# Performance work log

Hardware: AMD Instinct MI355X
Metric: run time of the kernel (lower is better)

The kernel has to match this reference:

```python
import jax, jax.numpy as jnp
import numpy as np

G, NPG = 2048, 512          # glimpses, points per glimpse
N0 = G * NPG                # 1,048,576 input points
CPG, CPG2 = 128, 32         # clusters per glimpse at level1/level2
M1, M2 = G * CPG, G * CPG2  # 262144, 65536


def _seg_mean_np(x, ids, m):
    cnt = np.bincount(ids, minlength=m).astype(np.float32)
    out = np.stack([np.bincount(ids, weights=x[:, d], minlength=m) for d in range(x.shape[1])], axis=1)
    return (out / np.maximum(cnt, 1.0)[:, None]).astype(np.float32)


def setup_inputs() -> dict:
    key = jax.random.key(0)
    ks = jax.random.split(key, 16)
    rng = np.random.default_rng(0)
    pos_np = (rng.random((N0, 3)) * 4.0).astype(np.float32)
    # voxel_mean_pool level 0: each point -> a cluster within its glimpse
    g_of_pt = np.arange(N0) // NPG
    out_index0 = (g_of_pt * CPG + rng.integers(0, CPG, N0)).astype(np.int64)
    pos1_np = _seg_mean_np(pos_np, out_index0, M1)
    g_of_c1 = np.arange(M1) // CPG
    out_index1 = (g_of_c1 * CPG2 + rng.integers(0, CPG2, M1)).astype(np.int64)
    pos2_np = _seg_mean_np(pos1_np, out_index1, M2)
    out_index2 = (np.arange(M2) // CPG2).astype(np.int64)  # glimpse id per level-2 point

    def w(k, shp, s=0.05):
        return jax.random.normal(k, shp, dtype=jnp.float32) * s

    return {
        "rgb": jax.random.normal(ks[0], (N0, 1), dtype=jnp.float32),
        "pos": jnp.asarray(pos_np), "pos1": jnp.asarray(pos1_np), "pos2": jnp.asarray(pos2_np),
        "out_index0": jnp.asarray(out_index0), "out_index1": jnp.asarray(out_index1),
        "out_index2": jnp.asarray(out_index2),
        "eps": jax.random.normal(ks[1], (G, 128), dtype=jnp.float32),
        # conv1: local (c_in=1 + 3 -> 16), global (16 -> 32)
        "W1l": w(ks[2], (4, 16)), "b1l": jnp.zeros(16), "W1g": w(ks[3], (16, 32)), "b1g": jnp.zeros(32),
        # conv2: (32+3 -> 64), (64 -> 128)
        "W2l": w(ks[4], (35, 64)), "b2l": jnp.zeros(64), "W2g": w(ks[5], (64, 128)), "b2g": jnp.zeros(128),
        # conv3: (128+3 -> 128), (128 -> 256)
        "W3l": w(ks[6], (131, 128)), "b3l": jnp.zeros(128), "W3g": w(ks[7], (128, 256)), "b3g": jnp.zeros(256),
        "Wlin": w(ks[8], (256, 256)), "blin": jnp.zeros(256),
    }


def _point_conv(x_in, pos_in, pos_out, out_index, Wl, bl, Wg, bg):
    # gather relative position of each input point w.r.t. its output center
    rel = pos_in - pos_out[out_index]                      # [E,3]
    h = jax.nn.celu(jnp.concatenate([x_in, rel], -1) @ Wl + bl)  # per-edge MLP
    m = pos_out.shape[0]
    cnt = jax.ops.segment_sum(jnp.ones((h.shape[0],), h.dtype), out_index, num_segments=m)
    agg = jax.ops.segment_sum(h, out_index, num_segments=m) / jnp.maximum(cnt, 1.0)[:, None]
    return agg @ Wg + bg


def reference(rgb, pos, pos1, pos2, out_index0, out_index1, out_index2, eps,
              W1l, b1l, W1g, b1g, W2l, b2l, W2g, b2g, W3l, b3l, W3g, b3g, Wlin, blin):
    f = rgb  # ar=False path: feature = rgb
    f = jax.nn.celu(_point_conv(f, pos, pos1, out_index0, W1l, b1l, W1g, b1g))   # [M1,32]
    f = jax.nn.celu(_point_conv(f, pos1, pos2, out_index1, W2l, b2l, W2g, b2g))  # [M2,128]
    centers = jnp.zeros((G, 3), f.dtype)  # pos_sample = zeros_like(glimpse__center)
    f = jax.nn.celu(_point_conv(f, pos2, centers, out_index2, W3l, b3l, W3g, b3g))  # [G,256]
    out = f @ Wlin + blin
    mu, sg = jnp.split(out, 2, axis=1)
    sigma = jax.nn.softplus(sg)  # to_sigma
    z = mu + sigma * eps         # Normal.rsample
    z_what, z_mask = jnp.split(z, 2, axis=1)
    return z_what, z_mask, mu, sigma, f
```

## Files before the change

### kernel.cpp

```cpp
#include <hip/hip_runtime.h>
#include <hip/hip_bf16.h>
#include <cstddef>

#define G_   2048
#define NPG_ 512
#define CPG_ 128
#define CPG2_ 32

#define OFF_ZW 0
#define OFF_ZM (G_*64)
#define OFF_MU (2*G_*64)
#define OFF_SG (2*G_*64 + G_*128)
#define OFF_F  (2*G_*64 + 2*G_*128)

typedef __attribute__((ext_vector_type(8))) short bf16x8;
typedef __attribute__((ext_vector_type(4))) float f32x4;

__device__ __forceinline__ float celu_f(float x)     { return x > 0.f ? x : __expf(x) - 1.f; }
__device__ __forceinline__ float softplus_f(float x) { return fmaxf(x, 0.f) + __logf(1.f + __expf(-fabsf(x))); }
__device__ __forceinline__ unsigned short f2bf(float x) {
    __hip_bfloat16 h = __float2bfloat16(x);
    return *reinterpret_cast<unsigned short*>(&h);
}
__device__ __forceinline__ float bflo(unsigned w) { return __uint_as_float(w << 16); }
__device__ __forceinline__ float bfhi(unsigned w) { return __uint_as_float(w & 0xffff0000u); }

__global__ void k_prep(const float* __restrict__ W2l, const float* __restrict__ W2g,
                       const float* __restrict__ W3l, const float* __restrict__ W3g,
                       const float* __restrict__ Wlin,
                       unsigned short* __restrict__ w2lT, unsigned short* __restrict__ w2gT,
                       unsigned short* __restrict__ w3lT, unsigned short* __restrict__ w3gT,
                       unsigned short* __restrict__ wlinT)
{
    const int tid = blockIdx.x*256 + threadIdx.x, stride = gridDim.x*256;
    for (int i = tid; i < 64*64; i += stride) {
        const int ch = i >> 6, k = i & 63;
        w2lT[i] = f2bf(k < 35 ? W2l[k*64 + ch] : 0.f);
    }
    for (int i = tid; i < 128*64; i += stride) {
        const int ch = i >> 6, k = i & 63;
        w2gT[i] = f2bf(W2g[k*128 + ch]);
    }
    for (int i = tid; i < 128*160; i += stride) {
        const int ch = i / 160, k = i % 160;
        w3lT[i] = f2bf(k < 131 ? W3l[k*128 + ch] : 0.f);
    }
    for (int i = tid; i < 256*128; i += stride) {
        const int ch = i >> 7, k = i & 127;
        w3gT[i] = f2bf(W3g[k*256 + ch]);
    }
    for (int i = tid; i < 256*256; i += stride) {
        const int ch = i >> 8, k = i & 255;
        wlinT[i] = f2bf(Wlin[k*256 + ch]);
    }
}

__global__ __launch_bounds__(256, 4) void k_fused(
    const float* __restrict__ rgb, const float* __restrict__ pos, const float* __restrict__ pos1,
    const float* __restrict__ pos2, const int* __restrict__ idx0, const int* __restrict__ idx1,
    const float* __restrict__ W1l, const float* __restrict__ b1l,
    const float* __restrict__ W1g, const float* __restrict__ b1g,
    const unsigned short* __restrict__ w2lT, const float* __restrict__ b2l,
    const unsigned short* __restrict__ w2gT, const float* __restrict__ b2g,
    const unsigned short* __restrict__ w3lT, const float* __restrict__ b3l,
    unsigned short* __restrict__ aggws)
{
    const int g = blockIdx.x, t = threadIdx.x;
    const int lane = t & 63, wv = t >> 6;
    const int lr = lane & 15, quad = lane >> 4;

    __shared__ __align__(16) unsigned char smem[39936];
    uint2* const spts = (uint2*)smem;
    unsigned short* const sT   = (unsigned short*)smem;
    unsigned short* const agg2 = (unsigned short*)smem;
    float* const red  = (float*)smem;
    float* const aggT = (float*)(smem + 8704);
    float* const sW1g = (float*)(smem + 16896);
    unsigned short* const xs3  = (unsigned short*)(smem + 8704);
    unsigned short* const xs16 = (unsigned short*)(smem + 19456);
    unsigned short* const HT   = xs16;
    int* const cnt   = (int*)(smem + 37888);
    int* const start = (int*)(smem + 38400);
    int* const ctr   = (int*)(smem + 38912);
    unsigned short* const slc = (unsigned short*)(smem + 39424);
    int* const cnti  = (int*)(smem + 39680);
    float* const invc = (float*)(smem + 39808);

    for (int i = t; i < 512; i += 256) sW1g[i] = W1g[i];
    if (t < CPG_) cnt[t] = 0;
    if (t < CPG2_) cnti[t] = 0;
    if (t < CPG_) {
        const int c2 = idx1[g*CPG_ + t];
        slc[t] = (unsigned short)(c2 - g*CPG2_);
        #pragma unroll
        for (int d = 0; d < 3; d++)
            xs16[t*72 + 32 + d] = f2bf(pos1[(g*CPG_ + t)*3 + d] - pos2[c2*3 + d]);
    }
    for (int i = t; i < 128*29; i += 256) {
        const int r = i / 29, c = 35 + (i - r*29);
        xs16[r*72 + c] = 0;
    }
    __syncthreads();

    float px0[2], prx[2], pry[2], prz[2];
    int plc[2];
    #pragma unroll
    for (int r = 0; r < 2; r++) {
        const int lp = r*256 + t;
        const int p  = g*NPG_ + lp;
        const int c  = idx0[p];
        plc[r] = c - g*CPG_;
        px0[r] = rgb[p];
        prx[r] = pos[p*3+0] - pos1[c*3+0];
        pry[r] = pos[p*3+1] - pos1[c*3+1];
        prz[r] = pos[p*3+2] - pos1[c*3+2];
        atomicAdd(&cnt[plc[r]], 1);
    }
    if (t < CPG_) atomicAdd(&cnti[slc[t]], 1);
    __syncthreads();

    if (t < CPG_) {
        int val = cnt[t];
        const int ln = t & 63;
        #pragma unroll
        for (int d = 1; d < 64; d <<= 1) {
            const int v = __shfl_up(val, d, 64);
            if (ln >= d) val += v;
        }
        ctr[t] = val;
    }
    __syncthreads();
    if (t >= 64 && t < CPG_) ctr[t] += ctr[63];
    __syncthreads();
    if (t < CPG_) { const int s = ctr[t] - cnt[t]; start[t] = s; ctr[t] = s; }
    if (t < CPG2_) invc[t] = 1.f / fmaxf((float)cnti[t], 1.f);
    __syncthreads();

    #pragma unroll
    for (int r = 0; r < 2; r++) {
        const int slot = atomicAdd(&ctr[plc[r]], 1);
        uint2 pk;
        pk.x = (unsigned)f2bf(px0[r]) | ((unsigned)f2bf(prx[r]) << 16);
        pk.y = (unsigned)f2bf(pry[r]) | ((unsigned)f2bf(prz[r]) << 16);
        spts[slot] = pk;
    }
    __syncthreads();

    {
        const int c = t >> 1, ch0 = (t & 1) * 8;
        float wj[8], wx[8], wy[8], wz[8], bb2[8];
        #pragma unroll
        for (int j = 0; j < 8; j++) {
            wj[j] = W1l[ch0+j]; wx[j] = W1l[16+ch0+j];
            wy[j] = W1l[32+ch0+j]; wz[j] = W1l[48+ch0+j];
            bb2[j] = b1l[ch0+j];
        }
        float a[8];
        #pragma unroll
        for (int j = 0; j < 8; j++) a[j] = 0.f;
        const int n = cnt[c], base = start[c];
        for (int i = 0; i < n; i++) {
            const uint2 pk = spts[base + i];
            const float x0 = bflo(pk.x), rx = bfhi(pk.x);
            const float ry = bflo(pk.y), rz = bfhi(pk.y);
            #pragma unroll
            for (int j = 0; j < 8; j++) {
                const float h = bb2[j] + x0*wj[j] + rx*wx[j] + ry*wy[j] + rz*wz[j];
                a[j] += celu_f(h);
            }
        }
        const float inv = 1.f / fmaxf((float)n, 1.f);
        #pragma unroll
        for (int j = 0; j < 8; j++) aggT[c*16 + ch0 + j] = a[j] * inv;
    }
    __syncthreads();

    {
        const int oc = t & 31;
        float wreg[16];
        #pragma unroll
        for (int j = 0; j < 16; j++) wreg[j] = sW1g[j*32 + oc];
        const float bg = b1g[oc];
        #pragma unroll
        for (int i = 0; i < 16; i++) {
            const int lc = (t >> 5) + i*8;
            float a = bg;
            #pragma unroll
            for (int j = 0; j < 16; j += 4) {
                const float4 a4 = *(const float4*)&aggT[lc*16 + j];
                a += a4.x*wreg[j] + a4.y*wreg[j+1] + a4.z*wreg[j+2] + a4.w*wreg[j+3];
            }
            xs16[lc*72 + oc] = f2bf(celu_f(a));
        }
    }
    for (int i = t; i < 1088; i += 256) ((uint2*)sT)[i] = make_uint2(0u, 0u);
    __syncthreads();
    if (t < CPG_) sT[slc[t]*136 + t] = 0x3F80;
    __syncthreads();

    float hv[8][4];
    {
        const int chn = wv*16 + lr;
        const bf16x8 bw0 = *(const bf16x8*)&w2lT[chn*64 + quad*8];
        const bf16x8 bw1 = *(const bf16x8*)&w2lT[chn*64 + 32 + quad*8];
        const float bias = b2l[chn];
        #pragma unroll
        for (int m = 0; m < 8; m++) {
            f32x4 acc = (f32x4){bias, bias, bias, bias};
            const bf16x8 a0 = *(const bf16x8*)&xs16[(m*16 + lr)*72 + quad*8];
            const bf16x8 a1 = *(const bf16x8*)&xs16[(m*16 + lr)*72 + 32 + quad*8];
            acc = __builtin_amdgcn_mfma_f32_16x16x32_bf16(a0, bw0, acc, 0, 0, 0);
            acc = __builtin_amdgcn_mfma_f32_16x16x32_bf16(a1, bw1, acc, 0, 0, 0);
            #pragma unroll
            for (int r = 0; r < 4; r++) hv[m][r] = celu_f(acc[r]);
        }
    }
    __syncthreads();

    {
        const int chn = wv*16 + lr;
        #pragma unroll
        for (int m = 0; m < 8; m++) {
            uint2 p;
            p.x = (unsigned)f2bf(hv[m][0]) | ((unsigned)f2bf(hv[m][1]) << 16);
            p.y = (unsigned)f2bf(hv[m][2]) | ((unsigned)f2bf(hv[m][3]) << 16);
            *(uint2*)&HT[chn*136 + m*16 + quad*4] = p;
        }
    }
    if (t < CPG2_) {
        #pragma unroll
        for (int d = 0; d < 3; d++)
            xs3[t*168 + 128 + d] = f2bf(pos2[(g*CPG2_ + t)*3 + d]);
    }
    for (int i = t; i < 32*29; i += 256) {
        const int r = i / 29, c = 131 + (i - r*29);
        xs3[r*168 + c] = 0;
    }
    __syncthreads();

    float aggv[2][4];
    {
        const int ch = wv*16 + lr;
        f32x4 acc[2];
        acc[0] = (f32x4){0.f, 0.f, 0.f, 0.f};
        acc[1] = (f32x4){0.f, 0.f, 0.f, 0.f};
        #pragma unroll
        for (int ks = 0; ks < 4; ks++) {
            const bf16x8 b = *(const bf16x8*)&HT[ch*136 + ks*32 + quad*8];
            #pragma unroll
            for (int mt = 0; mt < 2; mt++) {
                const bf16x8 a = *(const bf16x8*)&sT[(mt*16 + lr)*136 + ks*32 + quad*8];
                acc[mt] = __builtin_amdgcn_mfma_f32_16x16x32_bf16(a, b, acc[mt], 0, 0, 0);
            }
        }
        #pragma unroll
        for (int mt = 0; mt < 2; mt++)
        #pragma unroll
        for (int r = 0; r < 4; r++)
            aggv[mt][r] = acc[mt][r] * invc[mt*16 + quad*4 + r];
    }
    __syncthreads();

    {
        const int ch = wv*16 + lr;
        #pragma unroll
        for (int mt = 0; mt < 2; mt++)
        #pragma unroll
        for (int r = 0; r < 4; r++)
            agg2[(mt*16 + quad*4 + r)*72 + ch] = f2bf(aggv[mt][r]);
    }
    __syncthreads();

    {
        f32x4 acc2[2][2];
        int   chn2[2];
        bf16x8 bw[2][2];
        #pragma unroll
        for (int nt = 0; nt < 2; nt++) {
            chn2[nt] = (wv + nt*4)*16 + lr;
            const float bias = b2g[chn2[nt]];
            #pragma unroll
            for (int mt = 0; mt < 2; mt++) acc2[nt][mt] = (f32x4){bias, bias, bias, bias};
            bw[nt][0] = *(const bf16x8*)&w2gT[chn2[nt]*64 + quad*8];
            bw[nt][1] = *(const bf16x8*)&w2gT[chn2[nt]*64 + 32 + quad*8];
        }
        #pragma unroll
        for (int ks = 0; ks < 2; ks++) {
            #pragma unroll
            for (int mt = 0; mt < 2; mt++) {
                const bf16x8 a = *(const bf16x8*)&agg2[(mt*16 + lr)*72 + ks*32 + quad*8];
                acc2[0][mt] = __builtin_amdgcn_mfma_f32_16x16x32_bf16(a, bw[0][ks], acc2[0][mt], 0, 0, 0);
                acc2[1][mt] = __builtin_amdgcn_mfma_f32_16x16x32_bf16(a, bw[1][ks], acc2[1][mt], 0, 0, 0);
            }
        }
        #pragma unroll
        for (int nt = 0; nt < 2; nt++)
        #pragma unroll
        for (int mt = 0; mt < 2; mt++)
        #pragma unroll
        for (int r = 0; r < 4; r++) {
            const int row = mt*16 + quad*4 + r;
            xs3[row*168 + chn2[nt]] = f2bf(celu_f(acc2[nt][mt][r]));
        }
    }
    __syncthreads();

    {
        f32x4 acc[2][2];
        int chn[2];
        #pragma unroll
        for (int nt = 0; nt < 2; nt++) {
            chn[nt] = (wv + nt*4)*16 + lr;
            const float bias = b3l[chn[nt]];
            #pragma unroll
            for (int mt = 0; mt < 2; mt++) acc[nt][mt] = (f32x4){bias, bias, bias, bias};
        }
        #pragma unroll
        for (int ks = 0; ks < 5; ks++) {
            const bf16x8 b0 = *(const bf16x8*)&w3lT[chn[0]*160 + ks*32 + quad*8];
            const bf16x8 b1 = *(const bf16x8*)&w3lT[chn[1]*160 + ks*32 + quad*8];
            #pragma unroll
            for (int mt = 0; mt < 2; mt++) {
                const bf16x8 a = *(const bf16x8*)&xs3[(mt*16 + lr)*168 + ks*32 + quad*8];
                acc[0][mt] = __builtin_amdgcn_mfma_f32_16x16x32_bf16(a, b0, acc[0][mt], 0, 0, 0);
                acc[1][mt] = __builtin_amdgcn_mfma_f32_16x16x32_bf16(a, b1, acc[1][mt], 0, 0, 0);
            }
        }
        #pragma unroll
        for (int nt = 0; nt < 2; nt++)
        #pragma unroll
        for (int mt = 0; mt < 2; mt++) {
            const float p = celu_f(acc[nt][mt][0]) + celu_f(acc[nt][mt][1])
                          + celu_f(acc[nt][mt][2]) + celu_f(acc[nt][mt][3]);
            red[chn[nt]*9 + mt*4 + quad] = p;
        }
    }
    __syncthreads();

    if (t < 128) {
        const float* rp = &red[t*9];
        float a = 0.f;
        #pragma unroll
        for (int p = 0; p < 8; p++) a += rp[p];
        aggws[(size_t)g*128 + t] = f2bf(a * (1.f/32.f));
    }
}

__global__ __launch_bounds__(256) void k_head(
    const unsigned short* __restrict__ aggws,
    const unsigned short* __restrict__ w3gT, const float* __restrict__ b3g,
    const unsigned short* __restrict__ wlinT, const float* __restrict__ blin,
    const float* __restrict__ eps, float* __restrict__ out)
{
    const int g0 = blockIdx.x * 16, t = threadIdx.x;
    const int lane = t & 63, wv = t >> 6;
    const int lr = lane & 15, quad = lane >> 4;
    __shared__ __align__(16) unsigned short aggB[16*136];
    __shared__ __align__(16) unsigned short f3B[16*264];
    __shared__ float outs[16*260];

    {
        const int row = t >> 4, col8 = (t & 15) * 8;
        const uint4 v = ((const uint4*)aggws)[(size_t)g0*16 + t];
        *(uint4*)&aggB[row*136 + col8] = v;
    }
    __syncthreads();

    {
        f32x4 c3[4];
        int ch3[4];
        #pragma unroll
        for (int nt = 0; nt < 4; nt++) {
            ch3[nt] = (wv + nt*4)*16 + lr;
            const float bias = b3g[ch3[nt]];
            c3[nt] = (f32x4){bias, bias, bias, bias};
        }
        #pragma unroll
        for (int ks = 0; ks < 4; ks++) {
            const bf16x8 a = *(const bf16x8*)&aggB[lr*136 + ks*32 + quad*8];
            #pragma unroll
            for (int nt = 0; nt < 4; nt++) {
                const bf16x8 b = *(const bf16x8*)&w3gT[ch3[nt]*128 + ks*32 + quad*8];
                c3[nt] = __builtin_amdgcn_mfma_f32_16x16x32_bf16(a, b, c3[nt], 0, 0, 0);
            }
        }
        #pragma unroll
        for (int nt = 0; nt < 4; nt++)
        #pragma unroll
        for (int r = 0; r < 4; r++) {
            const int row = quad*4 + r;
            const float v = celu_f(c3[nt][r]);
            out[OFF_F + (size_t)(g0 + row)*256 + ch3[nt]] = v;
            f3B[row*264 + ch3[nt]] = f2bf(v);
        }
    }
    __syncthreads();

    {
        f32x4 cl[4];
        int ch4[4];
        #pragma unroll
        for (int nt = 0; nt < 4; nt++) {
            ch4[nt] = (wv + nt*4)*16 + lr;
            const float bias = blin[ch4[nt]];
            cl[nt] = (f32x4){bias, bias, bias, bias};
        }
        #pragma unroll
        for (int ks = 0; ks < 8; ks++) {
            const bf16x8 a = *(const bf16x8*)&f3B[lr*264 + ks*32 + quad*8];
            #pragma unroll
            for (int nt = 0; nt < 4; nt++) {
                const bf16x8 b = *(const bf16x8*)&wlinT[ch4[nt]*256 + ks*32 + quad*8];
                cl[nt] = __builtin_amdgcn_mfma_f32_16x16x32_bf16(a, b, cl[nt], 0, 0, 0);
            }
        }
        #pragma unroll
        for (int nt = 0; nt < 4; nt++)
        #pragma unroll
        for (int r = 0; r < 4; r++)
            outs[(quad*4 + r)*260 + ch4[nt]] = cl[nt][r];
    }
    __syncthreads();

    for (int i = t; i < 2048; i += 256) {
        const int gl = i >> 7, ch = i & 127;
        const int g = g0 + gl;
        const float mu    = outs[gl*260 + ch];
        const float sigma = softplus_f(outs[gl*260 + 128 + ch]);
        const float z     = mu + sigma * eps[g*128 + ch];
        out[OFF_MU + (size_t)g*128 + ch] = mu;
        out[OFF_SG + (size_t)g*128 + ch] = sigma;
        if (ch < 64) out[OFF_ZW + (size_t)g*64 + ch] = z;
        else         out[OFF_ZM + (size_t)g*64 + (ch - 64)] = z;
    }
}

extern "C" void kernel_launch(void* const* d_in, const int* in_sizes, int n_in,
                              void* d_out, int out_size, void* d_ws, size_t ws_size,
                              hipStream_t stream)
{
    const float* rgb  = (const float*)d_in[0];
    const float* pos  = (const float*)d_in[1];
    const float* pos1 = (const float*)d_in[2];
    const float* pos2 = (const float*)d_in[3];
    const int*   idx0 = (const int*)d_in[4];
    const int*   idx1 = (const int*)d_in[5];
    const float* eps  = (const float*)d_in[7];
    const float* W1l = (const float*)d_in[8],  *b1l = (const float*)d_in[9];
    const float* W1g = (const float*)d_in[10], *b1g = (const float*)d_in[11];
    const float* W2l = (const float*)d_in[12], *b2l = (const float*)d_in[13];
    const float* W2g = (const float*)d_in[14], *b2g = (const float*)d_in[15];
    const float* W3l = (const float*)d_in[16], *b3l = (const float*)d_in[17];
    const float* W3g = (const float*)d_in[18], *b3g = (const float*)d_in[19];
    const float* Wlin = (const float*)d_in[20], *blin = (const float*)d_in[21];

    unsigned short* w2lT  = (unsigned short*)d_ws;
    unsigned short* w2gT  = w2lT + 64*64;
    unsigned short* w3lT  = w2gT + 128*64;
    unsigned short* w3gT  = w3lT + 128*160;
    unsigned short* wlinT = w3gT + 256*128;
    unsigned short* aggws = wlinT + 256*256;
    float* outp = (float*)d_out;

    k_prep <<<64,    256, 0, stream>>>(W2l, W2g, W3l, W3g, Wlin, w2lT, w2gT, w3lT, w3gT, wlinT);
    k_fused<<<G_,    256, 0, stream>>>(rgb, pos, pos1, pos2, idx0, idx1,
                                       W1l, b1l, W1g, b1g,
                                       w2lT, b2l, w2gT, b2g, w3lT, b3l, aggws);
    k_head <<<G_/16, 256, 0, stream>>>(aggws, w3gT, b3g, wlinT, blin, eps, outp);
}
```

Baseline: 161.3 us.

## Shrink fused kernel LDS via MFMA level-1 global layer and buffer reuse

The conv1 global 16->32 linear layer is moved from scalar FP32 FMAs reading an LDS copy of W1g onto bf16 MFMA, using a pre-transposed, padded W1g written by the prep kernel. The level-1 aggregates are now stored as bf16 in LDS. The shared-memory map is rearranged so buffers alias more tightly, cutting LDS from about 39 KB to about 29 KB, and launch bounds rise to 5 blocks per CU to exploit the extra occupancy. A barrier in the prefix scan is merged away and zero-fills are rescheduled. The trade-offs are extra bf16 rounding of the level-1 features and register pressure under the tighter launch bound.

```diff
diff --git a/kernel.cpp b/kernel.cpp
--- a/kernel.cpp
+++ b/kernel.cpp
@@ -27,10 +27,10 @@
 
 __global__ void k_prep(const float* __restrict__ W2l, const float* __restrict__ W2g,
                        const float* __restrict__ W3l, const float* __restrict__ W3g,
-                       const float* __restrict__ Wlin,
+                       const float* __restrict__ Wlin, const float* __restrict__ W1g,
                        unsigned short* __restrict__ w2lT, unsigned short* __restrict__ w2gT,
                        unsigned short* __restrict__ w3lT, unsigned short* __restrict__ w3gT,
-                       unsigned short* __restrict__ wlinT)
+                       unsigned short* __restrict__ wlinT, unsigned short* __restrict__ w1gT)
 {
     const int tid = blockIdx.x*256 + threadIdx.x, stride = gridDim.x*256;
     for (int i = tid; i < 64*64; i += stride) {
@@ -53,13 +53,17 @@
         const int ch = i >> 8, k = i & 255;
         wlinT[i] = f2bf(Wlin[k*256 + ch]);
     }
+    for (int i = tid; i < 32*40; i += stride) {
+        const int ch = i / 40, k = i % 40;
+        w1gT[i] = f2bf(k < 16 ? W1g[k*32 + ch] : 0.f);
+    }
 }
 
-__global__ __launch_bounds__(256, 4) void k_fused(
+__global__ __launch_bounds__(256, 5) void k_fused(
     const float* __restrict__ rgb, const float* __restrict__ pos, const float* __restrict__ pos1,
     const float* __restrict__ pos2, const int* __restrict__ idx0, const int* __restrict__ idx1,
     const float* __restrict__ W1l, const float* __restrict__ b1l,
-    const float* __restrict__ W1g, const float* __restrict__ b1g,
+    const unsigned short* __restrict__ w1gT, const float* __restrict__ b1g,
     const unsigned short* __restrict__ w2lT, const float* __restrict__ b2l,
     const unsigned short* __restrict__ w2gT, const float* __restrict__ b2g,
     const unsigned short* __restrict__ w3lT, const float* __restrict__ b3l,
@@ -69,39 +73,40 @@
     const int lane = t & 63, wv = t >> 6;
     const int lr = lane & 15, quad = lane >> 4;
 
-    __shared__ __align__(16) unsigned char smem[39936];
+    __shared__ __align__(16) unsigned char smem[29184];
     uint2* const spts = (uint2*)smem;
-    unsigned short* const sT   = (unsigned short*)smem;
-    unsigned short* const agg2 = (unsigned short*)smem;
-    float* const red  = (float*)smem;
-    float* const aggT = (float*)(smem + 8704);
-    float* const sW1g = (float*)(smem + 16896);
-    unsigned short* const xs3  = (unsigned short*)(smem + 8704);
-    unsigned short* const xs16 = (unsigned short*)(smem + 19456);
-    unsigned short* const HT   = xs16;
-    int* const cnt   = (int*)(smem + 37888);
-    int* const start = (int*)(smem + 38400);
-    int* const ctr   = (int*)(smem + 38912);
-    unsigned short* const slc = (unsigned short*)(smem + 39424);
-    int* const cnti  = (int*)(smem + 39680);
-    float* const invc = (float*)(smem + 39808);
-
-    for (int i = t; i < 512; i += 256) sW1g[i] = W1g[i];
+    unsigned short* const aggT = (unsigned short*)(smem + 4096);
+    unsigned short* const xs16 = (unsigned short*)smem;
+    unsigned short* const HT   = (unsigned short*)smem;
+    unsigned short* const xs3  = (unsigned short*)smem;
+    unsigned short* const sT   = (unsigned short*)(smem + 18432);
+    unsigned short* const agg2 = (unsigned short*)(smem + 18432);
+    float* const red  = (float*)(smem + 18432);
+    int* const cnt   = (int*)(smem + 27136);
+    int* const start = (int*)(smem + 27648);
+    int* const ctr   = (int*)(smem + 28160);
+    unsigned short* const slc = (unsigned short*)(smem + 28672);
+    int* const cnti  = (int*)(smem + 28928);
+    float* const invc = (float*)(smem + 29056);
+
     if (t < CPG_) cnt[t] = 0;
     if (t < CPG2_) cnti[t] = 0;
+    float relx = 0.f, rely = 0.f, relz = 0.f;
     if (t < CPG_) {
         const int c2 = idx1[g*CPG_ + t];
         slc[t] = (unsigned short)(c2 - g*CPG2_);
-        #pragma unroll
-        for (int d = 0; d < 3; d++)
-            xs16[t*72 + 32 + d] = f2bf(pos1[(g*CPG_ + t)*3 + d] - pos2[c2*3 + d]);
-    }
-    for (int i = t; i < 128*29; i += 256) {
-        const int r = i / 29, c = 35 + (i - r*29);
-        xs16[r*72 + c] = 0;
-    }
-    __syncthreads();
-
+        relx = pos1[(g*CPG_ + t)*3 + 0] - pos2[c2*3 + 0];
+        rely = pos1[(g*CPG_ + t)*3 + 1] - pos2[c2*3 + 1];
+        relz = pos1[(g*CPG_ + t)*3 + 2] - pos2[c2*3 + 2];
+    }
+    for (int i = t; i < 2176; i += 256) ((unsigned*)sT)[i] = 0u;
+    for (int i = t; i < 128*8; i += 256) {
+        const int r = i >> 3, j = i & 7;
+        ((unsigned*)aggT)[r*20 + 8 + j] = 0u;
+    }
+    __syncthreads();
+
+    if (t < CPG_) sT[slc[t]*136 + t] = 0x3F80;
     float px0[2], prx[2], pry[2], prz[2];
     int plc[2];
     #pragma unroll
@@ -130,9 +135,12 @@
         ctr[t] = val;
     }
     __syncthreads();
-    if (t >= 64 && t < CPG_) ctr[t] += ctr[63];
-    __syncthreads();
-    if (t < CPG_) { const int s = ctr[t] - cnt[t]; start[t] = s; ctr[t] = s; }
+    if (t < CPG_) {
+        int v = ctr[t];
+        if (t >= 64) v += ctr[63];
+        const int s = v - cnt[t];
+        start[t] = s; ctr[t] = s;
+    }
     if (t < CPG2_) invc[t] = 1.f / fmaxf((float)cnti[t], 1.f);
     __syncthreads();
 
@@ -170,32 +178,53 @@
             }
         }
         const float inv = 1.f / fmaxf((float)n, 1.f);
-        #pragma unroll
-        for (int j = 0; j < 8; j++) aggT[c*16 + ch0 + j] = a[j] * inv;
-    }
-    __syncthreads();
-
-    {
-        const int oc = t & 31;
-        float wreg[16];
-        #pragma unroll
-        for (int j = 0; j < 16; j++) wreg[j] = sW1g[j*32 + oc];
-        const float bg = b1g[oc];
-        #pragma unroll
-        for (int i = 0; i < 16; i++) {
-            const int lc = (t >> 5) + i*8;
-            float a = bg;
-            #pragma unroll
-            for (int j = 0; j < 16; j += 4) {
-                const float4 a4 = *(const float4*)&aggT[lc*16 + j];
-                a += a4.x*wreg[j] + a4.y*wreg[j+1] + a4.z*wreg[j+2] + a4.w*wreg[j+3];
-            }
-            xs16[lc*72 + oc] = f2bf(celu_f(a));
-        }
-    }
-    for (int i = t; i < 1088; i += 256) ((uint2*)sT)[i] = make_uint2(0u, 0u);
-    __syncthreads();
-    if (t < CPG_) sT[slc[t]*136 + t] = 0x3F80;
+        uint2 q0, q1;
+        q0.x = (unsigned)f2bf(a[0]*inv) | ((unsigned)f2bf(a[1]*inv) << 16);
+        q0.y = (unsigned)f2bf(a[2]*inv) | ((unsigned)f2bf(a[3]*inv) << 16);
+        q1.x = (unsigned)f2bf(a[4]*inv) | ((unsigned)f2bf(a[5]*inv) << 16);
+        q1.y = (unsigned)f2bf(a[6]*inv) | ((unsigned)f2bf(a[7]*inv) << 16);
+        *(uint2*)&aggT[c*40 + ch0]     = q0;
+        *(uint2*)&aggT[c*40 + ch0 + 4] = q1;
+    }
+    __syncthreads();
+
+    f32x4 c1[2][2];
+    {
+        #pragma unroll
+        for (int nt = 0; nt < 2; nt++) {
+            const float bias = b1g[nt*16 + lr];
+            c1[nt][0] = (f32x4){bias, bias, bias, bias};
+            c1[nt][1] = (f32x4){bias, bias, bias, bias};
+        }
+        const bf16x8 b0 = *(const bf16x8*)&w1gT[(0*16 + lr)*40 + quad*8];
+        const bf16x8 b1 = *(const bf16x8*)&w1gT[(1*16 + lr)*40 + quad*8];
+        #pragma unroll
+        for (int mt = 0; mt < 2; mt++) {
+            const bf16x8 a = *(const bf16x8*)&aggT[((2*wv + mt)*16 + lr)*40 + quad*8];
+            c1[0][mt] = __builtin_amdgcn_mfma_f32_16x16x32_bf16(a, b0, c1[0][mt], 0, 0, 0);
+            c1[1][mt] = __builtin_amdgcn_mfma_f32_16x16x32_bf16(a, b1, c1[1][mt], 0, 0, 0);
+        }
+    }
+    __syncthreads();
+
+    #pragma unroll
+    for (int nt = 0; nt < 2; nt++)
+    #pragma unroll
+    for (int mt = 0; mt < 2; mt++)
+    #pragma unroll
+    for (int r = 0; r < 4; r++) {
+        const int cl = (2*wv + mt)*16 + quad*4 + r;
+        xs16[cl*72 + nt*16 + lr] = f2bf(celu_f(c1[nt][mt][r]));
+    }
+    if (t < CPG_) {
+        xs16[t*72 + 32] = f2bf(relx);
+        xs16[t*72 + 33] = f2bf(rely);
+        xs16[t*72 + 34] = f2bf(relz);
+    }
+    for (int i = t; i < 128*29; i += 256) {
+        const int r = i / 29, c = 35 + (i - r*29);
+        xs16[r*72 + c] = 0;
+    }
     __syncthreads();
 
     float hv[8][4];
@@ -227,15 +256,6 @@
             *(uint2*)&HT[chn*136 + m*16 + quad*4] = p;
         }
     }
-    if (t < CPG2_) {
-        #pragma unroll
-        for (int d = 0; d < 3; d++)
-            xs3[t*168 + 128 + d] = f2bf(pos2[(g*CPG2_ + t)*3 + d]);
-    }
-    for (int i = t; i < 32*29; i += 256) {
-        const int r = i / 29, c = 131 + (i - r*29);
-        xs3[r*168 + c] = 0;
-    }
     __syncthreads();
 
     float aggv[2][4];
@@ -268,6 +288,15 @@
         #pragma unroll
         for (int r = 0; r < 4; r++)
             agg2[(mt*16 + quad*4 + r)*72 + ch] = f2bf(aggv[mt][r]);
+    }
+    if (t < CPG2_) {
+        #pragma unroll
+        for (int d = 0; d < 3; d++)
+            xs3[t*168 + 128 + d] = f2bf(pos2[(g*CPG2_ + t)*3 + d]);
+    }
+    for (int i = t; i < 32*29; i += 256) {
+        const int r = i / 29, c = 131 + (i - r*29);
+        xs3[r*168 + c] = 0;
     }
     __syncthreads();
 
@@ -459,12 +488,14 @@
     unsigned short* w3lT  = w2gT + 128*64;
     unsigned short* w3gT  = w3lT + 128*160;
     unsigned short* wlinT = w3gT + 256*128;
-    unsigned short* aggws = wlinT + 256*256;
+    unsigned short* w1gT  = wlinT + 256*256;
+    unsigned short* aggws = w1gT + 32*40;
     float* outp = (float*)d_out;
 
-    k_prep <<<64,    256, 0, stream>>>(W2l, W2g, W3l, W3g, Wlin, w2lT, w2gT, w3lT, w3gT, wlinT);
+    k_prep <<<64,    256, 0, stream>>>(W2l, W2g, W3l, W3g, Wlin, W1g,
+                                       w2lT, w2gT, w3lT, w3gT, wlinT, w1gT);
     k_fused<<<G_,    256, 0, stream>>>(rgb, pos, pos1, pos2, idx0, idx1,
-                                       W1l, b1l, W1g, b1g,
+                                       W1l, b1l, w1gT, b1g,
                                        w2lT, b2l, w2gT, b2g, w3lT, b3l, aggws);
     k_head <<<G_/16, 256, 0, stream>>>(aggws, w3gT, b3g, wlinT, blin, eps, outp);
 }
```

After: 158.4 us. Within noise of the previous version (-1.8%).
